# Performance work log

Measured on AMD Instinct MI355X. Metric: run time of the kernel, lower is better.

The kernel has to match this reference:

```python
import jax, jax.numpy as jnp
import numpy as np


def setup_inputs() -> dict:
    key = jax.random.key(0)
    ks = jax.random.split(key, 6)
    B, S, H, F, E = 4, 2048, 1024, 4096, 8
    x = jax.random.normal(ks[0], (B, S, H), dtype=jnp.float32)
    Wr = jax.random.normal(ks[1], (H, E), dtype=jnp.float32) * (1.0 / np.sqrt(H))
    br = jnp.zeros((E,), dtype=jnp.float32)
    W1 = jax.random.normal(ks[2], (E, H, F), dtype=jnp.float32) * (1.0 / np.sqrt(H))
    b1 = jnp.zeros((E, F), dtype=jnp.float32)
    W2 = jax.random.normal(ks[3], (E, F, H), dtype=jnp.float32) * (1.0 / np.sqrt(F))
    b2 = jnp.zeros((E, H), dtype=jnp.float32)
    b_buf = jnp.zeros((E,), dtype=jnp.float32)  # load-balancing bias buffer, zero-init
    return {"x": x, "b_buf": b_buf, "Wr": Wr, "br": br,
            "W1": W1, "b1": b1, "W2": W2, "b2": b2, "k": 2}


def reference(x, b_buf, Wr, br, W1, b1, W2, b2, k):
    # Router
    scores = jnp.einsum('bsh,he->bse', x, Wr) + br          # [B,S,E]
    probs = jax.nn.softmax(scores, axis=-1)
    # load_balancing: expert selection uses biased scores (b_buf pre-update)
    _, expert_id = jax.lax.top_k(probs + b_buf, k)          # [B,S,k] int
    # combine weights use unbiased probs
    p, _ = jax.lax.top_k(probs, k)                          # [B,S,k]
    # Dense-dispatch reference: run every expert MLP on all tokens,
    # then select via one-hot mask (same math as gather/scatter dispatch).
    h1 = jnp.einsum('bsh,ehf->ebsf', x, W1) + b1[:, None, None, :]
    h1 = jax.nn.gelu(h1, approximate=False)                 # torch nn.GELU = exact
    out_e = jnp.einsum('ebsf,efh->ebsh', h1, W2) + b2[:, None, None, :]
    E = W1.shape[0]
    onehot = (expert_id[None, :, :, :] == jnp.arange(E)[:, None, None, None]).astype(x.dtype)  # [E,B,S,k]
    out_k = jnp.einsum('ebsk,ebsh->bskh', onehot, out_e)    # scatter-combine per slot
    w = p / jnp.sum(p, axis=-1, keepdims=True)              # normalize top-k probs
    return jnp.einsum('bsk,bskh->bsh', w, out_k)
```

## Files before the change

### kernel.cpp

```cpp
#include <hip/hip_runtime.h>
#include <stdint.h>

#define NTOK 8192
#define H_ 1024
#define F_ 4096
#define E_ 8
#define VCAP 18432
#define VMBLK 72
#define MT 144
#define NCOMP 16384

using f32x4  = __attribute__((ext_vector_type(4))) float;
using short8 = __attribute__((ext_vector_type(8))) short;

typedef __attribute__((address_space(1))) const uint32_t gu32;
typedef __attribute__((address_space(3))) uint32_t lu32;

__device__ __forceinline__ void glds16(const void* g, void* l) {
  __builtin_amdgcn_global_load_lds((gu32*)g, (lu32*)l, 16, 0, 0);
}

__device__ __forceinline__ ushort f2bf(float f) {
  union { float f; uint32_t u; } v; v.f = f;
  uint32_t r = (v.u + 0x7FFFu + ((v.u >> 16) & 1u)) >> 16;
  return (ushort)r;
}

__device__ __forceinline__ float gelu_t(float x) {
  float u = 0.7978845608028654f * (x + 0.044715f * x * x * x);
  float e = exp2f(u * 2.885390081777927f);
  float th = 1.0f - 2.0f / (1.0f + e);
  return 0.5f * x * (1.0f + th);
}

__global__ __launch_bounds__(256) void k_transcvt2(const float* __restrict__ W1,
                                                   const float* __restrict__ W2,
                                                   ushort* __restrict__ W1T,
                                                   ushort* __restrict__ W2T,
                                                   int* cnt, int* cur, int* tok,
                                                   float* wl, int* v2c) {
  int bid = blockIdx.x;
  if (bid < VMBLK) {
    int i = bid * 256 + threadIdx.x;
    if (i < E_) { cnt[i] = 0; cur[i] = 0; }
    if (i < VCAP) { tok[i] = -1; wl[i] = 0.f; v2c[i] = -1; }
  }
  const float* W; ushort* WT; int R, C, nx, t;
  if (bid < 8192) { W = W1; WT = W1T; R = 1024; C = 4096; nx = 64; t = bid; }
  else            { W = W2; WT = W2T; R = 4096; C = 1024; nx = 16; t = bid - 8192; }
  int e = t >> 10, r = t & 1023;
  int c0 = (r % nx) * 64, r0 = (r / nx) * 64;

  __shared__ float tb[64][65];
  const float* Wp = W + (size_t)e * R * C;
  ushort* Tp = WT + (size_t)e * R * C;
  int tx = threadIdx.x & 15, ty = threadIdx.x >> 4;
#pragma unroll
  for (int i = 0; i < 4; i++) {
    int lr = ty + i * 16;
    const float4 v = *(const float4*)&Wp[(size_t)(r0 + lr) * C + c0 + tx * 4];
    tb[lr][tx * 4 + 0] = v.x; tb[lr][tx * 4 + 1] = v.y;
    tb[lr][tx * 4 + 2] = v.z; tb[lr][tx * 4 + 3] = v.w;
  }
  __syncthreads();
#pragma unroll
  for (int i = 0; i < 4; i++) {
    int lc = ty + i * 16;
    ushort4 o;
    o.x = f2bf(tb[tx * 4 + 0][lc]);
    o.y = f2bf(tb[tx * 4 + 1][lc]);
    o.z = f2bf(tb[tx * 4 + 2][lc]);
    o.w = f2bf(tb[tx * 4 + 3][lc]);
    *(ushort4*)&Tp[(size_t)(c0 + lc) * R + r0 + tx * 4] = o;
  }
}

__global__ __launch_bounds__(256) void k_router(const float* __restrict__ x,
                                                const float* __restrict__ Wr,
                                                const float* __restrict__ br,
                                                const float* __restrict__ bbuf,
                                                int* cnt, int* te, float* tw) {
  int wid = threadIdx.x >> 6, lane = threadIdx.x & 63;
  int t = blockIdx.x * 4 + wid;
  const float* xp = x + (size_t)t * H_;
  double acc[E_];
#pragma unroll
  for (int e = 0; e < E_; e++) acc[e] = 0.0;
  for (int j = lane; j < H_; j += 64) {
    float xv = xp[j];
    const float4 w0 = *(const float4*)&Wr[j * 8];
    const float4 w1 = *(const float4*)&Wr[j * 8 + 4];
    acc[0] += (double)xv * (double)w0.x;
    acc[1] += (double)xv * (double)w0.y;
    acc[2] += (double)xv * (double)w0.z;
    acc[3] += (double)xv * (double)w0.w;
    acc[4] += (double)xv * (double)w1.x;
    acc[5] += (double)xv * (double)w1.y;
    acc[6] += (double)xv * (double)w1.z;
    acc[7] += (double)xv * (double)w1.w;
  }
#pragma unroll
  for (int e = 0; e < E_; e++)
    for (int s = 32; s > 0; s >>= 1) acc[e] += __shfl_xor(acc[e], s);
  if (lane == 0) {
    double s[E_], m = -1e300;
    for (int e = 0; e < E_; e++) { s[e] = acc[e] + (double)br[e]; if (s[e] > m) m = s[e]; }
    double pe[E_], sum = 0.0;
    for (int e = 0; e < E_; e++) { pe[e] = exp(s[e] - m); sum += pe[e]; }
    double pr[E_], bb[E_];
    for (int e = 0; e < E_; e++) { pr[e] = pe[e] / sum; bb[e] = pr[e] + (double)bbuf[e]; }
    int e0 = 0;
    for (int e = 1; e < E_; e++) if (bb[e] > bb[e0]) e0 = e;
    int e1 = (e0 == 0) ? 1 : 0;
    for (int e = 0; e < E_; e++) if (e != e0 && bb[e] > bb[e1]) e1 = e;
    int a0 = 0;
    for (int e = 1; e < E_; e++) if (pr[e] > pr[a0]) a0 = e;
    int a1 = (a0 == 0) ? 1 : 0;
    for (int e = 0; e < E_; e++) if (e != a0 && pr[e] > pr[a1]) a1 = e;
    double iv = 1.0 / (pr[a0] + pr[a1]);
    te[t * 2] = e0; te[t * 2 + 1] = e1;
    tw[t * 2] = (float)(pr[a0] * iv); tw[t * 2 + 1] = (float)(pr[a1] * iv);
    atomicAdd(&cnt[e0], 1); atomicAdd(&cnt[e1], 1);
  }
}

__global__ void k_offsets(const int* cnt, int* off, int* coff) {
  if (threadIdx.x == 0 && blockIdx.x == 0) {
    int o = 0, c = 0;
    for (int e = 0; e < E_; e++) {
      off[e] = o; coff[e] = c;
      o += ((cnt[e] + 255) >> 8) << 8;
      c += cnt[e];
    }
    off[E_] = o; coff[E_] = c;
  }
}

__global__ void k_build(const int* __restrict__ te, const float* __restrict__ tw,
                        const int* __restrict__ off, const int* __restrict__ coff,
                        int* cur, int* tok, float* wl, int* v2c, int* ctok) {
  int t = blockIdx.x * 256 + threadIdx.x;
  if (t >= NTOK) return;
#pragma unroll
  for (int s = 0; s < 2; s++) {
    int e = te[t * 2 + s];
    int slot = atomicAdd(&cur[e], 1);
    int vp = off[e] + slot;
    int cp = coff[e] + slot;
    tok[vp] = t; wl[vp] = tw[t * 2 + s]; v2c[vp] = cp; ctok[cp] = t;
  }
}

__global__ __launch_bounds__(256) void k_gather(const float* __restrict__ x,
                                                const int* __restrict__ ctok,
                                                ushort* __restrict__ Xg,
                                                float* __restrict__ out) {
  int gid = blockIdx.x * 256 + threadIdx.x;
  if (gid < NTOK * H_ / 4) {
    float4 z; z.x = 0.f; z.y = 0.f; z.z = 0.f; z.w = 0.f;
    ((float4*)out)[gid] = z;
  }
  int row = blockIdx.x;
  int t = ctok[row];
  const float4* src = (const float4*)(x + (size_t)t * H_);
  ushort4* dst = (ushort4*)(Xg + (size_t)row * H_);
  int i = threadIdx.x;
  float4 v = src[i];
  ushort4 o; o.x = f2bf(v.x); o.y = f2bf(v.y); o.z = f2bf(v.z); o.w = f2bf(v.w);
  dst[i] = o;
}

template <int MODE>
__global__ __launch_bounds__(256, 3) void k_gemm(const ushort* __restrict__ A,
                                                 const ushort* __restrict__ BT,
                                                 const float* __restrict__ bias,
                                                 ushort* __restrict__ h1,
                                                 float* __restrict__ Out,
                                                 const int* __restrict__ off,
                                                 const int* __restrict__ v2c,
                                                 const int* __restrict__ tok,
                                                 const float* __restrict__ wl,
                                                 int K, int N, int NTe) {
  __shared__ __align__(16) ushort As[128 * 64];
  __shared__ __align__(16) ushort Bs[128 * 64];

  int nwg = gridDim.x;
  int cpx = nwg >> 3;
  int bid = blockIdx.x;
  int lid = (bid & 7) * cpx + (bid >> 3);
  int ng = lid / (MT * 8), r = lid % (MT * 8);
  int m = r >> 3;
  int ne = (ng << 3) + (r & 7);
  int row0 = m << 7;
  if (row0 >= off[E_]) return;
  int e = 0;
  while (off[e + 1] <= row0) e++;
  int n0, k0, nk;
  if (MODE == 0) { n0 = ne << 7; k0 = 0; nk = K >> 6; }
  else           { n0 = (ne & 7) << 7; k0 = (ne >> 3) * (K >> 1); nk = K >> 7; }
  const ushort* Bp = BT + (size_t)e * (size_t)N * (size_t)K;

  int tid = threadIdx.x, lane = tid & 63, w = tid >> 6;
  int wr = w >> 1, wc = w & 1;

  f32x4 acc[4][4];
#pragma unroll
  for (int mm = 0; mm < 4; mm++)
#pragma unroll
    for (int nn = 0; nn < 4; nn++) acc[mm][nn] = (f32x4){0.f, 0.f, 0.f, 0.f};

  int urow = (w << 3) + (lane >> 3);
  int sc = (lane & 7) ^ (urow & 7);
  const char *aP0, *aP1, *aP2, *aP3, *bP0, *bP1, *bP2, *bP3;
  {
    size_t kb = (size_t)k0 * 2 + (size_t)sc * 16;
    int c0 = v2c[row0 + 0 * 32 + urow];  if (c0 < 0) c0 = 0;
    int c1 = v2c[row0 + 1 * 32 + urow];  if (c1 < 0) c1 = 0;
    int c2 = v2c[row0 + 2 * 32 + urow];  if (c2 < 0) c2 = 0;
    int c3 = v2c[row0 + 3 * 32 + urow];  if (c3 < 0) c3 = 0;
    aP0 = (const char*)(A + (size_t)c0 * K) + kb;
    aP1 = (const char*)(A + (size_t)c1 * K) + kb;
    aP2 = (const char*)(A + (size_t)c2 * K) + kb;
    aP3 = (const char*)(A + (size_t)c3 * K) + kb;
    bP0 = (const char*)(Bp + (size_t)(n0 + 0 * 32 + urow) * K) + kb;
    bP1 = (const char*)(Bp + (size_t)(n0 + 1 * 32 + urow) * K) + kb;
    bP2 = (const char*)(Bp + (size_t)(n0 + 2 * 32 + urow) * K) + kb;
    bP3 = (const char*)(Bp + (size_t)(n0 + 3 * 32 + urow) * K) + kb;
  }

  int fr = lane & 15, fq = lane >> 4;
  int frs = fr & 7;

  for (int kk = 0; kk < nk; ++kk) {
    size_t kbo = (size_t)kk * 128;
    if (kk) __syncthreads();
    glds16(aP0 + kbo, (char*)As + 0 * 4096 + (w << 10));
    glds16(bP0 + kbo, (char*)Bs + 0 * 4096 + (w << 10));
    glds16(aP1 + kbo, (char*)As + 1 * 4096 + (w << 10));
    glds16(bP1 + kbo, (char*)Bs + 1 * 4096 + (w << 10));
    glds16(aP2 + kbo, (char*)As + 2 * 4096 + (w << 10));
    glds16(bP2 + kbo, (char*)Bs + 2 * 4096 + (w << 10));
    glds16(aP3 + kbo, (char*)As + 3 * 4096 + (w << 10));
    glds16(bP3 + kbo, (char*)Bs + 3 * 4096 + (w << 10));
    __syncthreads();
#pragma unroll
    for (int ks = 0; ks < 2; ++ks) {
      short8 af[4], bf[4];
      int kc = (((ks << 2) + fq) ^ frs) << 3;
#pragma unroll
      for (int i = 0; i < 4; ++i)
        af[i] = *(const short8*)&As[((wr << 6) + i * 16 + fr) * 64 + kc];
#pragma unroll
      for (int i = 0; i < 4; ++i)
        bf[i] = *(const short8*)&Bs[((wc << 6) + i * 16 + fr) * 64 + kc];
#pragma unroll
      for (int mm = 0; mm < 4; ++mm)
#pragma unroll
        for (int nn = 0; nn < 4; ++nn)
          acc[mm][nn] = __builtin_amdgcn_mfma_f32_16x16x32_bf16(af[mm], bf[nn], acc[mm][nn], 0, 0, 0);
    }
  }

  const float* bp = bias + (size_t)e * N;
  int cb = n0 + (wc << 6);
  if (MODE == 0) {
#pragma unroll
    for (int mm = 0; mm < 4; mm++) {
#pragma unroll
      for (int j = 0; j < 4; j++) {
        int vr = row0 + (wr << 6) + mm * 16 + (fq << 2) + j;
        int cr = v2c[vr];
        if (cr < 0) continue;
        ushort* hp = h1 + (size_t)cr * N + cb;
#pragma unroll
        for (int nn = 0; nn < 4; nn++) {
          float v = acc[mm][nn][j] + bp[cb + nn * 16 + fr];
          hp[nn * 16 + fr] = f2bf(gelu_t(v));
        }
      }
    }
  } else {
    bool addb = (k0 == 0);
#pragma unroll
    for (int mm = 0; mm < 4; mm++) {
#pragma unroll
      for (int j = 0; j < 4; j++) {
        int vr = row0 + (wr << 6) + mm * 16 + (fq << 2) + j;
        int t2 = tok[vr];
        if (t2 < 0) continue;
        float wgt = wl[vr];
#pragma unroll
        for (int nn = 0; nn < 4; nn++) {
          int c = cb + nn * 16 + fr;
          float v = acc[mm][nn][j] + (addb ? bp[c] : 0.f);
          atomicAdd(&Out[(size_t)t2 * (size_t)N + c], wgt * v);
        }
      }
    }
  }
}

extern "C" void kernel_launch(void* const* d_in, const int* in_sizes, int n_in,
                              void* d_out, int out_size, void* d_ws, size_t ws_size,
                              hipStream_t stream) {
  (void)in_sizes; (void)n_in; (void)out_size; (void)ws_size;
  const float* x    = (const float*)d_in[0];
  const float* bbuf = (const float*)d_in[1];
  const float* Wr   = (const float*)d_in[2];
  const float* br   = (const float*)d_in[3];
  const float* W1   = (const float*)d_in[4];
  const float* b1   = (const float*)d_in[5];
  const float* W2   = (const float*)d_in[6];
  const float* b2   = (const float*)d_in[7];
  float* out = (float*)d_out;

  char* ws = (char*)d_ws;
  ushort* W1T = (ushort*)ws;
  ushort* W2T = (ushort*)(ws + 67108864);
  ushort* Xg  = (ushort*)(ws + 134217728);
  ushort* h1  = (ushort*)(ws + 167772160);
  char* meta  = ws + 301989888;
  int*   cnt  = (int*)(meta);
  int*   off  = (int*)(meta + 64);
  int*   coff = (int*)(meta + 128);
  int*   cur  = (int*)(meta + 192);
  int*   te   = (int*)(meta + 256);
  float* tw   = (float*)(meta + 65792);
  int*   tok  = (int*)(meta + 131328);
  float* wl   = (float*)(meta + 205056);
  int*   v2c  = (int*)(meta + 278784);
  int*   ctok = (int*)(meta + 352512);

  k_transcvt2<<<16384, 256, 0, stream>>>(W1, W2, W1T, W2T, cnt, cur, tok, wl, v2c);
  k_router<<<NTOK / 4, 256, 0, stream>>>(x, Wr, br, bbuf, cnt, te, tw);
  k_offsets<<<1, 64, 0, stream>>>(cnt, off, coff);
  k_build<<<NTOK / 256, 256, 0, stream>>>(te, tw, off, coff, cur, tok, wl, v2c, ctok);
  k_gather<<<NCOMP, 256, 0, stream>>>(x, ctok, Xg, out);
  k_gemm<0><<<32 * MT, 256, 0, stream>>>(Xg, W1T, b1, h1, nullptr,
                                         off, v2c, nullptr, nullptr,
                                         H_, F_, 32);
  k_gemm<1><<<16 * MT, 256, 0, stream>>>(h1, W2T, b2, nullptr, out,
                                         off, v2c, tok, wl,
                                         F_, H_, 16);
}
```

Baseline: 876.8 us.

## Enlarge expert GEMM row tile to 256 and fuse router into prep kernel

The grouped expert GEMMs now use a 256x128 output tile. Each wave holds an 8x4 grid of MFMA accumulators, and the A shared-memory buffer is doubled. This halves how often each weight tile is reloaded and removes half the blocks, in exchange for lower occupancy: the launch bound drops from 3 to 2 and register pressure rises. The router computation is also merged into the weight-transpose/init kernel as extra blocks, saving a launch. Those router blocks use atomics on counters that are zeroed by other blocks of the same kernel, so correctness relies on block dispatch order.

After: 995.7 us. 13.6% more time.

```diff
diff --git a/kernel.cpp b/kernel.cpp
--- a/kernel.cpp
+++ b/kernel.cpp
@@ -7,7 +7,6 @@
 #define E_ 8
 #define VCAP 18432
 #define VMBLK 72
-#define MT 144
 #define NCOMP 16384
 
 using f32x4  = __attribute__((ext_vector_type(4))) float;
@@ -33,17 +32,67 @@
   return 0.5f * x * (1.0f + th);
 }
 
-__global__ __launch_bounds__(256) void k_transcvt2(const float* __restrict__ W1,
-                                                   const float* __restrict__ W2,
-                                                   ushort* __restrict__ W1T,
-                                                   ushort* __restrict__ W2T,
-                                                   int* cnt, int* cur, int* tok,
-                                                   float* wl, int* v2c) {
+__global__ __launch_bounds__(256) void k_prep(const float* __restrict__ W1,
+                                              const float* __restrict__ W2,
+                                              ushort* __restrict__ W1T,
+                                              ushort* __restrict__ W2T,
+                                              const float* __restrict__ x,
+                                              const float* __restrict__ Wr,
+                                              const float* __restrict__ br,
+                                              const float* __restrict__ bbuf,
+                                              int* cnt, int* te, float* tw,
+                                              int* cur, int* tok, float* wl,
+                                              int* v2c) {
   int bid = blockIdx.x;
   if (bid < VMBLK) {
     int i = bid * 256 + threadIdx.x;
     if (i < E_) { cnt[i] = 0; cur[i] = 0; }
     if (i < VCAP) { tok[i] = -1; wl[i] = 0.f; v2c[i] = -1; }
+  }
+  if (bid >= 16384) {
+    int wid = threadIdx.x >> 6, lane = threadIdx.x & 63;
+    int t = (bid - 16384) * 4 + wid;
+    const float* xp = x + (size_t)t * H_;
+    double acc[E_];
+#pragma unroll
+    for (int e = 0; e < E_; e++) acc[e] = 0.0;
+    for (int j = lane; j < H_; j += 64) {
+      float xv = xp[j];
+      const float4 w0 = *(const float4*)&Wr[j * 8];
+      const float4 w1 = *(const float4*)&Wr[j * 8 + 4];
+      acc[0] += (double)xv * (double)w0.x;
+      acc[1] += (double)xv * (double)w0.y;
+      acc[2] += (double)xv * (double)w0.z;
+      acc[3] += (double)xv * (double)w0.w;
+      acc[4] += (double)xv * (double)w1.x;
+      acc[5] += (double)xv * (double)w1.y;
+      acc[6] += (double)xv * (double)w1.z;
+      acc[7] += (double)xv * (double)w1.w;
+    }
+#pragma unroll
+    for (int e = 0; e < E_; e++)
+      for (int s = 32; s > 0; s >>= 1) acc[e] += __shfl_xor(acc[e], s);
+    if (lane == 0) {
+      double s[E_], m = -1e300;
+      for (int e = 0; e < E_; e++) { s[e] = acc[e] + (double)br[e]; if (s[e] > m) m = s[e]; }
+      double pe[E_], sum = 0.0;
+      for (int e = 0; e < E_; e++) { pe[e] = exp(s[e] - m); sum += pe[e]; }
+      double pr[E_], bb[E_];
+      for (int e = 0; e < E_; e++) { pr[e] = pe[e] / sum; bb[e] = pr[e] + (double)bbuf[e]; }
+      int e0 = 0;
+      for (int e = 1; e < E_; e++) if (bb[e] > bb[e0]) e0 = e;
+      int e1 = (e0 == 0) ? 1 : 0;
+      for (int e = 0; e < E_; e++) if (e != e0 && bb[e] > bb[e1]) e1 = e;
+      int a0 = 0;
+      for (int e = 1; e < E_; e++) if (pr[e] > pr[a0]) a0 = e;
+      int a1 = (a0 == 0) ? 1 : 0;
+      for (int e = 0; e < E_; e++) if (e != a0 && pr[e] > pr[a1]) a1 = e;
+      double iv = 1.0 / (pr[a0] + pr[a1]);
+      te[t * 2] = e0; te[t * 2 + 1] = e1;
+      tw[t * 2] = (float)(pr[a0] * iv); tw[t * 2 + 1] = (float)(pr[a1] * iv);
+      atomicAdd(&cnt[e0], 1); atomicAdd(&cnt[e1], 1);
+    }
+    return;
   }
   const float* W; ushort* WT; int R, C, nx, t;
   if (bid < 8192) { W = W1; WT = W1T; R = 1024; C = 4096; nx = 64; t = bid; }
@@ -75,55 +124,6 @@
   }
 }
 
-__global__ __launch_bounds__(256) void k_router(const float* __restrict__ x,
-                                                const float* __restrict__ Wr,
-                                                const float* __restrict__ br,
-                                                const float* __restrict__ bbuf,
-                                                int* cnt, int* te, float* tw) {
-  int wid = threadIdx.x >> 6, lane = threadIdx.x & 63;
-  int t = blockIdx.x * 4 + wid;
-  const float* xp = x + (size_t)t * H_;
-  double acc[E_];
-#pragma unroll
-  for (int e = 0; e < E_; e++) acc[e] = 0.0;
-  for (int j = lane; j < H_; j += 64) {
-    float xv = xp[j];
-    const float4 w0 = *(const float4*)&Wr[j * 8];
-    const float4 w1 = *(const float4*)&Wr[j * 8 + 4];
-    acc[0] += (double)xv * (double)w0.x;
-    acc[1] += (double)xv * (double)w0.y;
-    acc[2] += (double)xv * (double)w0.z;
-    acc[3] += (double)xv * (double)w0.w;
-    acc[4] += (double)xv * (double)w1.x;
-    acc[5] += (double)xv * (double)w1.y;
-    acc[6] += (double)xv * (double)w1.z;
-    acc[7] += (double)xv * (double)w1.w;
-  }
-#pragma unroll
-  for (int e = 0; e < E_; e++)
-    for (int s = 32; s > 0; s >>= 1) acc[e] += __shfl_xor(acc[e], s);
-  if (lane == 0) {
-    double s[E_], m = -1e300;
-    for (int e = 0; e < E_; e++) { s[e] = acc[e] + (double)br[e]; if (s[e] > m) m = s[e]; }
-    double pe[E_], sum = 0.0;
-    for (int e = 0; e < E_; e++) { pe[e] = exp(s[e] - m); sum += pe[e]; }
-    double pr[E_], bb[E_];
-    for (int e = 0; e < E_; e++) { pr[e] = pe[e] / sum; bb[e] = pr[e] + (double)bbuf[e]; }
-    int e0 = 0;
-    for (int e = 1; e < E_; e++) if (bb[e] > bb[e0]) e0 = e;
-    int e1 = (e0 == 0) ? 1 : 0;
-    for (int e = 0; e < E_; e++) if (e != e0 && bb[e] > bb[e1]) e1 = e;
-    int a0 = 0;
-    for (int e = 1; e < E_; e++) if (pr[e] > pr[a0]) a0 = e;
-    int a1 = (a0 == 0) ? 1 : 0;
-    for (int e = 0; e < E_; e++) if (e != a0 && pr[e] > pr[a1]) a1 = e;
-    double iv = 1.0 / (pr[a0] + pr[a1]);
-    te[t * 2] = e0; te[t * 2 + 1] = e1;
-    tw[t * 2] = (float)(pr[a0] * iv); tw[t * 2 + 1] = (float)(pr[a1] * iv);
-    atomicAdd(&cnt[e0], 1); atomicAdd(&cnt[e1], 1);
-  }
-}
-
 __global__ void k_offsets(const int* cnt, int* off, int* coff) {
   if (threadIdx.x == 0 && blockIdx.x == 0) {
     int o = 0, c = 0;
@@ -171,7 +171,7 @@
 }
 
 template <int MODE>
-__global__ __launch_bounds__(256, 3) void k_gemm(const ushort* __restrict__ A,
+__global__ __launch_bounds__(256, 2) void k_gemm(const ushort* __restrict__ A,
                                                  const ushort* __restrict__ BT,
                                                  const float* __restrict__ bias,
                                                  ushort* __restrict__ h1,
@@ -181,17 +181,17 @@
                                                  const int* __restrict__ tok,
                                                  const float* __restrict__ wl,
                                                  int K, int N, int NTe) {
-  __shared__ __align__(16) ushort As[128 * 64];
+  __shared__ __align__(16) ushort As[256 * 64];
   __shared__ __align__(16) ushort Bs[128 * 64];
 
   int nwg = gridDim.x;
   int cpx = nwg >> 3;
   int bid = blockIdx.x;
   int lid = (bid & 7) * cpx + (bid >> 3);
-  int ng = lid / (MT * 8), r = lid % (MT * 8);
+  int ng = lid / (VMBLK * 8), r = lid % (VMBLK * 8);
   int m = r >> 3;
   int ne = (ng << 3) + (r & 7);
-  int row0 = m << 7;
+  int row0 = m << 8;
   if (row0 >= off[E_]) return;
   int e = 0;
   while (off[e + 1] <= row0) e++;
@@ -203,29 +203,40 @@
   int tid = threadIdx.x, lane = tid & 63, w = tid >> 6;
   int wr = w >> 1, wc = w & 1;
 
-  f32x4 acc[4][4];
-#pragma unroll
-  for (int mm = 0; mm < 4; mm++)
+  f32x4 acc[8][4];
+#pragma unroll
+  for (int mm = 0; mm < 8; mm++)
 #pragma unroll
     for (int nn = 0; nn < 4; nn++) acc[mm][nn] = (f32x4){0.f, 0.f, 0.f, 0.f};
 
-  int urow = (w << 3) + (lane >> 3);
-  int sc = (lane & 7) ^ (urow & 7);
-  const char *aP0, *aP1, *aP2, *aP3, *bP0, *bP1, *bP2, *bP3;
+  int urow = lane >> 3;
+  int sc = (lane & 7) ^ urow;
+  const char *aS0, *aS1, *aS2, *aS3, *aS4, *aS5, *aS6, *aS7;
+  const char *bS0, *bS1, *bS2, *bS3;
   {
     size_t kb = (size_t)k0 * 2 + (size_t)sc * 16;
-    int c0 = v2c[row0 + 0 * 32 + urow];  if (c0 < 0) c0 = 0;
-    int c1 = v2c[row0 + 1 * 32 + urow];  if (c1 < 0) c1 = 0;
-    int c2 = v2c[row0 + 2 * 32 + urow];  if (c2 < 0) c2 = 0;
-    int c3 = v2c[row0 + 3 * 32 + urow];  if (c3 < 0) c3 = 0;
-    aP0 = (const char*)(A + (size_t)c0 * K) + kb;
-    aP1 = (const char*)(A + (size_t)c1 * K) + kb;
-    aP2 = (const char*)(A + (size_t)c2 * K) + kb;
-    aP3 = (const char*)(A + (size_t)c3 * K) + kb;
-    bP0 = (const char*)(Bp + (size_t)(n0 + 0 * 32 + urow) * K) + kb;
-    bP1 = (const char*)(Bp + (size_t)(n0 + 1 * 32 + urow) * K) + kb;
-    bP2 = (const char*)(Bp + (size_t)(n0 + 2 * 32 + urow) * K) + kb;
-    bP3 = (const char*)(Bp + (size_t)(n0 + 3 * 32 + urow) * K) + kb;
+    int base = row0 + (w << 6) + urow;
+    int c0 = v2c[base + 0];  if (c0 < 0) c0 = 0;
+    int c1 = v2c[base + 8];  if (c1 < 0) c1 = 0;
+    int c2 = v2c[base + 16]; if (c2 < 0) c2 = 0;
+    int c3 = v2c[base + 24]; if (c3 < 0) c3 = 0;
+    int c4 = v2c[base + 32]; if (c4 < 0) c4 = 0;
+    int c5 = v2c[base + 40]; if (c5 < 0) c5 = 0;
+    int c6 = v2c[base + 48]; if (c6 < 0) c6 = 0;
+    int c7 = v2c[base + 56]; if (c7 < 0) c7 = 0;
+    aS0 = (const char*)(A + (size_t)c0 * K) + kb;
+    aS1 = (const char*)(A + (size_t)c1 * K) + kb;
+    aS2 = (const char*)(A + (size_t)c2 * K) + kb;
+    aS3 = (const char*)(A + (size_t)c3 * K) + kb;
+    aS4 = (const char*)(A + (size_t)c4 * K) + kb;
+    aS5 = (const char*)(A + (size_t)c5 * K) + kb;
+    aS6 = (const char*)(A + (size_t)c6 * K) + kb;
+    aS7 = (const char*)(A + (size_t)c7 * K) + kb;
+    int bb = n0 + (w << 5) + urow;
+    bS0 = (const char*)(Bp + (size_t)(bb + 0) * K) + kb;
+    bS1 = (const char*)(Bp + (size_t)(bb + 8) * K) + kb;
+    bS2 = (const char*)(Bp + (size_t)(bb + 16) * K) + kb;
+    bS3 = (const char*)(Bp + (size_t)(bb + 24) * K) + kb;
   }
 
   int fr = lane & 15, fq = lane >> 4;
@@ -234,27 +245,31 @@
   for (int kk = 0; kk < nk; ++kk) {
     size_t kbo = (size_t)kk * 128;
     if (kk) __syncthreads();
-    glds16(aP0 + kbo, (char*)As + 0 * 4096 + (w << 10));
-    glds16(bP0 + kbo, (char*)Bs + 0 * 4096 + (w << 10));
-    glds16(aP1 + kbo, (char*)As + 1 * 4096 + (w << 10));
-    glds16(bP1 + kbo, (char*)Bs + 1 * 4096 + (w << 10));
-    glds16(aP2 + kbo, (char*)As + 2 * 4096 + (w << 10));
-    glds16(bP2 + kbo, (char*)Bs + 2 * 4096 + (w << 10));
-    glds16(aP3 + kbo, (char*)As + 3 * 4096 + (w << 10));
-    glds16(bP3 + kbo, (char*)Bs + 3 * 4096 + (w << 10));
+    glds16(aS0 + kbo, (char*)As + (w << 13) + 0 * 1024);
+    glds16(aS1 + kbo, (char*)As + (w << 13) + 1 * 1024);
+    glds16(aS2 + kbo, (char*)As + (w << 13) + 2 * 1024);
+    glds16(aS3 + kbo, (char*)As + (w << 13) + 3 * 1024);
+    glds16(aS4 + kbo, (char*)As + (w << 13) + 4 * 1024);
+    glds16(aS5 + kbo, (char*)As + (w << 13) + 5 * 1024);
+    glds16(aS6 + kbo, (char*)As + (w << 13) + 6 * 1024);
+    glds16(aS7 + kbo, (char*)As + (w << 13) + 7 * 1024);
+    glds16(bS0 + kbo, (char*)Bs + (w << 12) + 0 * 1024);
+    glds16(bS1 + kbo, (char*)Bs + (w << 12) + 1 * 1024);
+    glds16(bS2 + kbo, (char*)Bs + (w << 12) + 2 * 1024);
+    glds16(bS3 + kbo, (char*)Bs + (w << 12) + 3 * 1024);
     __syncthreads();
 #pragma unroll
     for (int ks = 0; ks < 2; ++ks) {
-      short8 af[4], bf[4];
+      short8 af[8], bf[4];
       int kc = (((ks << 2) + fq) ^ frs) << 3;
 #pragma unroll
-      for (int i = 0; i < 4; ++i)
-        af[i] = *(const short8*)&As[((wr << 6) + i * 16 + fr) * 64 + kc];
+      for (int i = 0; i < 8; ++i)
+        af[i] = *(const short8*)&As[((wr << 7) + i * 16 + fr) * 64 + kc];
 #pragma unroll
       for (int i = 0; i < 4; ++i)
         bf[i] = *(const short8*)&Bs[((wc << 6) + i * 16 + fr) * 64 + kc];
 #pragma unroll
-      for (int mm = 0; mm < 4; ++mm)
+      for (int mm = 0; mm < 8; ++mm)
 #pragma unroll
         for (int nn = 0; nn < 4; ++nn)
           acc[mm][nn] = __builtin_amdgcn_mfma_f32_16x16x32_bf16(af[mm], bf[nn], acc[mm][nn], 0, 0, 0);
@@ -265,10 +280,10 @@
   int cb = n0 + (wc << 6);
   if (MODE == 0) {
 #pragma unroll
-    for (int mm = 0; mm < 4; mm++) {
+    for (int mm = 0; mm < 8; mm++) {
 #pragma unroll
       for (int j = 0; j < 4; j++) {
-        int vr = row0 + (wr << 6) + mm * 16 + (fq << 2) + j;
+        int vr = row0 + (wr << 7) + mm * 16 + (fq << 2) + j;
         int cr = v2c[vr];
         if (cr < 0) continue;
         ushort* hp = h1 + (size_t)cr * N + cb;
@@ -282,10 +297,10 @@
   } else {
     bool addb = (k0 == 0);
 #pragma unroll
-    for (int mm = 0; mm < 4; mm++) {
+    for (int mm = 0; mm < 8; mm++) {
 #pragma unroll
       for (int j = 0; j < 4; j++) {
-        int vr = row0 + (wr << 6) + mm * 16 + (fq << 2) + j;
+        int vr = row0 + (wr << 7) + mm * 16 + (fq << 2) + j;
         int t2 = tok[vr];
         if (t2 < 0) continue;
         float wgt = wl[vr];
@@ -331,15 +346,15 @@
   int*   v2c  = (int*)(meta + 278784);
   int*   ctok = (int*)(meta + 352512);
 
-  k_transcvt2<<<16384, 256, 0, stream>>>(W1, W2, W1T, W2T, cnt, cur, tok, wl, v2c);
-  k_router<<<NTOK / 4, 256, 0, stream>>>(x, Wr, br, bbuf, cnt, te, tw);
+  k_prep<<<18432, 256, 0, stream>>>(W1, W2, W1T, W2T, x, Wr, br, bbuf,
+                                    cnt, te, tw, cur, tok, wl, v2c);
   k_offsets<<<1, 64, 0, stream>>>(cnt, off, coff);
   k_build<<<NTOK / 256, 256, 0, stream>>>(te, tw, off, coff, cur, tok, wl, v2c, ctok);
   k_gather<<<NCOMP, 256, 0, stream>>>(x, ctok, Xg, out);
-  k_gemm<0><<<32 * MT, 256, 0, stream>>>(Xg, W1T, b1, h1, nullptr,
-                                         off, v2c, nullptr, nullptr,
-                                         H_, F_, 32);
-  k_gemm<1><<<16 * MT, 256, 0, stream>>>(h1, W2T, b2, nullptr, out,
-                                         off, v2c, tok, wl,
-                                         F_, H_, 16);
-}
+  k_gemm<0><<<32 * VMBLK, 256, 0, stream>>>(Xg, W1T, b1, h1, nullptr,
+                                            off, v2c, nullptr, nullptr,
+                                            H_, F_, 32);
+  k_gemm<1><<<16 * VMBLK, 256, 0, stream>>>(h1, W2T, b2, nullptr, out,
+                                            off, v2c, tok, wl,
+                                            F_, H_, 16);
+}
```
